# Performance work log

Hardware: AMD Instinct MI355X
Metric: run time of the kernel (lower is better)

## Reference

```python
import jax, jax.numpy as jnp
import numpy as np

NUM_HEADS = 4
OUTPUT_DIM = 64


def setup_inputs() -> dict:
    key = jax.random.key(0)
    k1, k2, k3 = jax.random.split(key, 3)
    B, N, F = 8, 2048, 256
    features = jax.random.normal(k1, (B, N, F), dtype=jnp.float32)
    adj_matrix = jax.random.uniform(k2, (B, N, N), dtype=jnp.float32)
    # learned params (glorot-ish scale)
    kernel = jax.random.normal(k3, (F, OUTPUT_DIM * NUM_HEADS), dtype=jnp.float32) * (1.0 / np.sqrt(F))
    bias = jnp.zeros((OUTPUT_DIM * NUM_HEADS,), dtype=jnp.float32)
    return {"features": features, "adj_matrix": adj_matrix, "kernel": kernel, "bias": bias}


def reference(features, adj_matrix, kernel, bias):
    B, N, F = features.shape
    H, D = NUM_HEADS, OUTPUT_DIM
    Wh = jnp.matmul(features, kernel)                 # [B, N, H*D]
    Whh = Wh.reshape(B, N, H, D)                      # [B, N, H, D]
    # per-node, per-head score: inner product Wh1 @ Wh2 = ||Wh||^2
    e = jnp.sum(Whh * Whh, axis=-1)                   # [B, N, H]
    attention = jax.nn.softmax(e, axis=1)             # softmax over nodes
    attention = jnp.mean(attention, axis=2)           # head mean -> [B, N]
    # adjacency mask (broadcast column score over neighbors)
    A = attention[:, :, None] * adj_matrix            # [B, N, N]
    out = jnp.matmul(A, Wh) + bias                    # [B, N, H*D]
    return jax.nn.relu(out)
```

## Files before the change

### kernel.cpp

```cpp
#include <hip/hip_runtime.h>
#include <hip/hip_bf16.h>

#define BATCH 8
#define NNODE 2048
#define FDIM 256
#define HD 256
#define NH 4
#define MROWS (BATCH*NNODE)

typedef float f32x4 __attribute__((ext_vector_type(4)));
typedef short s16x8 __attribute__((ext_vector_type(8)));
typedef unsigned short ushort_t;

#define MFMA __builtin_amdgcn_mfma_f32_16x16x32_bf16
#define SCHED0() __builtin_amdgcn_sched_barrier(0)
#define SBAR() __builtin_amdgcn_s_barrier()

__device__ __forceinline__ ushort_t f2bf(float f) {
    unsigned u = __builtin_bit_cast(unsigned, f);
    u += 0x7fffu + ((u >> 16) & 1u);
    return (ushort_t)(u >> 16);
}
__device__ __forceinline__ void split2(float f, ushort_t& h, ushort_t& l) {
    unsigned u = __builtin_bit_cast(unsigned, f);
    h = (ushort_t)(u >> 16);
    float fh = __builtin_bit_cast(float, u & 0xffff0000u);
    float lo = f - fh;
    l = (ushort_t)(__builtin_bit_cast(unsigned, lo) >> 16);
}

#define GLOAD16(gp, lp) __builtin_amdgcn_global_load_lds( \
    (const __attribute__((address_space(1))) void*)(gp),  \
    (__attribute__((address_space(3))) void*)(lp), 16, 0, 0)

__global__ __launch_bounds__(256) void wprep_kernel(
    const float* __restrict__ Wm,
    ushort_t* __restrict__ wt_hi, ushort_t* __restrict__ wt_lo)
{
    const int nn = blockIdx.x, k = threadIdx.x;
    ushort_t h, l;
    split2(Wm[(size_t)k * HD + nn], h, l);
    wt_hi[nn * FDIM + k] = h;
    wt_lo[nn * FDIM + k] = l;
}

__global__ __launch_bounds__(256, 4) void gemm1_kernel(
    const float* __restrict__ features,
    const ushort_t* __restrict__ wt_hi,
    const ushort_t* __restrict__ wt_lo,
    ushort_t* __restrict__ WhT_hi,
    ushort_t* __restrict__ WhT_lo,
    float* __restrict__ e_out)
{
    __shared__ __align__(16) ushort_t Ah[64 * 64];
    __shared__ __align__(16) ushort_t Al[64 * 64];
    __shared__ __align__(16) ushort_t Bh[64 * 64];
    __shared__ __align__(16) ushort_t Bl[64 * 64];
    __shared__ float red[64][2];

    const int tid = threadIdx.x, lane = tid & 63, w = tid >> 6;
    const int wr = w >> 1, wc = w & 1;
    const int row0 = blockIdx.x * 64;
    const int head = blockIdx.y;
    const int col0 = head * 64;

    const float* Ab = features + (size_t)row0 * FDIM;
    const ushort_t* Bhg = wt_hi + (size_t)col0 * FDIM;
    const ushort_t* Blg = wt_lo + (size_t)col0 * FDIM;

    const int sr0 = tid >> 3;
    const int sg8 = tid & 7;
    const int bc = (lane >> 3);
    const int bs = lane & 7;

    f32x4 ar[4];
    f32x4 acc[2][2];
    #pragma unroll
    for (int m = 0; m < 2; ++m)
        #pragma unroll
        for (int n = 0; n < 2; ++n) acc[m][n] = (f32x4)0.f;

    #define G1_LOADA(K0) do {                                                  \
        _Pragma("unroll")                                                      \
        for (int i = 0; i < 2; ++i) {                                          \
            const int r = sr0 + 32 * i;                                        \
            ar[2*i]   = *(const f32x4*)&Ab[(size_t)r * FDIM + (K0) + sg8 * 8]; \
            ar[2*i+1] = *(const f32x4*)&Ab[(size_t)r * FDIM + (K0) + sg8 * 8 + 4]; \
        }                                                                      \
    } while (0)

    #define G1_STAGEA() do {                                                   \
        _Pragma("unroll")                                                      \
        for (int i = 0; i < 2; ++i) {                                          \
            const int r = sr0 + 32 * i;                                        \
            s16x8 vh, vl; ushort_t hh, ll;                                     \
            _Pragma("unroll")                                                  \
            for (int j = 0; j < 4; ++j) {                                      \
                split2(ar[2*i][j], hh, ll);  vh[j] = (short)hh; vl[j] = (short)ll; \
            }                                                                  \
            _Pragma("unroll")                                                  \
            for (int j = 0; j < 4; ++j) {                                      \
                split2(ar[2*i+1][j], hh, ll); vh[4+j] = (short)hh; vl[4+j] = (short)ll; \
            }                                                                  \
            const int off = r * 64 + ((sg8 ^ (r & 7)) << 3);                   \
            *(s16x8*)&Ah[off] = vh; *(s16x8*)&Al[off] = vl;                    \
        }                                                                      \
    } while (0)

    #define G1_STAGEB(K0) do {                                                 \
        _Pragma("unroll")                                                      \
        for (int qq = 0; qq < 2; ++qq) {                                       \
            const int q = w + qq * 4;                                          \
            const int c = q * 8 + bc;                                          \
            const int g = bs ^ (c & 7);                                        \
            GLOAD16(&Bhg[(size_t)c * FDIM + (K0) + g * 8], &Bh[q * 512]);      \
            GLOAD16(&Blg[(size_t)c * FDIM + (K0) + g * 8], &Bl[q * 512]);      \
        }                                                                      \
    } while (0)

    G1_LOADA(0);
    for (int t = 0; t < 4; ++t) {
        G1_STAGEB(t * 64);
        G1_STAGEA();
        if (t < 3) G1_LOADA((t + 1) * 64);
        if (t < 3) { asm volatile("s_waitcnt lgkmcnt(0) vmcnt(4)" ::: "memory"); }
        else       { asm volatile("s_waitcnt lgkmcnt(0) vmcnt(0)" ::: "memory"); }
        SCHED0(); SBAR(); SCHED0();
        #pragma unroll
        for (int kh = 0; kh < 2; ++kh) {
            const int kg = kh * 4 + (lane >> 4);
            s16x8 afh[2], afl[2], bfh[2], bfl[2];
            #pragma unroll
            for (int m = 0; m < 2; ++m) {
                const int r = wr * 32 + m * 16 + (lane & 15);
                const int off = r * 64 + ((kg ^ (r & 7)) << 3);
                afh[m] = *(const s16x8*)&Ah[off];
                afl[m] = *(const s16x8*)&Al[off];
            }
            #pragma unroll
            for (int n = 0; n < 2; ++n) {
                const int c = wc * 32 + n * 16 + (lane & 15);
                const int off = c * 64 + ((kg ^ (c & 7)) << 3);
                bfh[n] = *(const s16x8*)&Bh[off];
                bfl[n] = *(const s16x8*)&Bl[off];
            }
            #pragma unroll
            for (int m = 0; m < 2; ++m)
                #pragma unroll
                for (int n = 0; n < 2; ++n) {
                    acc[m][n] = MFMA(afh[m], bfh[n], acc[m][n], 0, 0, 0);
                    acc[m][n] = MFMA(afh[m], bfl[n], acc[m][n], 0, 0, 0);
                    acc[m][n] = MFMA(afl[m], bfh[n], acc[m][n], 0, 0, 0);
                }
        }
        SCHED0(); SBAR(); SCHED0();
    }

    #pragma unroll
    for (int m = 0; m < 2; ++m)
        #pragma unroll
        for (int j = 0; j < 4; ++j) {
            float p = acc[m][0][j] * acc[m][0][j] + acc[m][1][j] * acc[m][1][j];
            p += __shfl_xor(p, 1, 64);
            p += __shfl_xor(p, 2, 64);
            p += __shfl_xor(p, 4, 64);
            p += __shfl_xor(p, 8, 64);
            if ((lane & 15) == 0)
                red[wr * 32 + m * 16 + (lane >> 4) * 4 + j][wc] = p;
        }

    __syncthreads();
    ushort_t* Th = Ah;
    ushort_t* Tl = Al;
    #pragma unroll
    for (int m = 0; m < 2; ++m)
        #pragma unroll
        for (int n = 0; n < 2; ++n)
            #pragma unroll
            for (int j = 0; j < 4; ++j) {
                const int rr = wr * 32 + m * 16 + (lane >> 4) * 4 + j;
                const int cc = wc * 32 + n * 16 + (lane & 15);
                const int ad = cc * 64 + ((((rr >> 3) ^ (cc & 7))) << 3) + (rr & 7);
                ushort_t hh, ll;
                split2(acc[m][n][j], hh, ll);
                Th[ad] = hh; Tl[ad] = ll;
            }
    __syncthreads();

    if (tid < 64) {
        const int rg = row0 + tid;
        e_out[((size_t)((rg >> 11) * NH + head)) * NNODE + (rg & 2047)] =
            red[tid][0] + red[tid][1];
    }
    const int bb = row0 >> 11, node0 = row0 & 2047;
    #pragma unroll
    for (int i = 0; i < 2; ++i) {
        const int gid = tid + 256 * i;
        const int c = gid >> 3, gr = gid & 7;
        const int ad = c * 64 + ((gr ^ (c & 7)) << 3);
        uint4 vh = *(const uint4*)&Th[ad];
        uint4 vl = *(const uint4*)&Tl[ad];
        const size_t o = ((size_t)bb * HD + col0 + c) * NNODE + node0 + gr * 8;
        *(uint4*)&WhT_hi[o] = vh;
        *(uint4*)&WhT_lo[o] = vl;
    }
}

__global__ __launch_bounds__(256) void sm_kernel(
    const float* __restrict__ e, float* __restrict__ ms)
{
    __shared__ float red[8];
    const int bh = blockIdx.x, tid = threadIdx.x;
    const int lane = tid & 63, w = tid >> 6;
    const float* row = e + (size_t)bh * NNODE;
    float mx = -3.0e38f;
    for (int n = tid; n < NNODE; n += 256) mx = fmaxf(mx, row[n]);
    #pragma unroll
    for (int off = 32; off; off >>= 1) mx = fmaxf(mx, __shfl_xor(mx, off, 64));
    if (lane == 0) red[w] = mx;
    __syncthreads();
    mx = fmaxf(fmaxf(red[0], red[1]), fmaxf(red[2], red[3]));
    float s = 0.f;
    for (int n = tid; n < NNODE; n += 256) s += expf(row[n] - mx);
    #pragma unroll
    for (int off = 32; off; off >>= 1) s += __shfl_xor(s, off, 64);
    if (lane == 0) red[4 + w] = s;
    __syncthreads();
    if (tid == 0) {
        ms[bh * 2] = mx;
        ms[bh * 2 + 1] = red[4] + red[5] + red[6] + red[7];
    }
}

__global__ __launch_bounds__(256) void att_kernel(
    const float* __restrict__ e, const float* __restrict__ ms,
    float* __restrict__ attv)
{
    const int i = blockIdx.x * 256 + threadIdx.x;
    const int b = i >> 11, n = i & 2047;
    float a = 0.f;
    #pragma unroll
    for (int h = 0; h < NH; ++h) {
        const int bh = b * NH + h;
        a += expf(e[(size_t)bh * NNODE + n] - ms[bh * 2]) / ms[bh * 2 + 1];
    }
    attv[i] = 0.25f * a;
}

__global__ __launch_bounds__(256, 2) void gemm2_kernel(
    const float* __restrict__ adj,
    const ushort_t* __restrict__ WhT_hi,
    const ushort_t* __restrict__ WhT_lo,
    const float* __restrict__ att,
    const float* __restrict__ bias,
    float* __restrict__ out)
{
    __shared__ __align__(16) ushort_t Bh[3][64 * 64];
    __shared__ __align__(16) ushort_t Bl[3][64 * 64];

    const int tid = threadIdx.x, lane = tid & 63, w = tid >> 6;

    const int bid = blockIdx.x;
    const int wg = (bid & 7) * 64 + (bid >> 3);
    const int bx = wg & 15, by = (wg >> 4) & 3, b = wg >> 6;
    const int row0 = bx * 128, col0 = by * 64;

    const ushort_t* Bhg = WhT_hi + ((size_t)b * HD + col0) * NNODE;
    const ushort_t* Blg = WhT_lo + ((size_t)b * HD + col0) * NNODE;

    const float* pA = adj + (size_t)b * NNODE * NNODE
                    + (size_t)(row0 + w * 32 + (lane & 15)) * NNODE
                    + ((lane >> 4) * 8);

    const int bc = lane >> 3, bs = lane & 7;

    f32x4 ar[2][2][2];
    s16x8 afh[2][2];
    f32x4 acc[2][4];
    #pragma unroll
    for (int m = 0; m < 2; ++m)
        #pragma unroll
        for (int n = 0; n < 4; ++n) acc[m][n] = (f32x4)0.f;

    #define G2_LOADA(K0) do {                                                   \
        _Pragma("unroll")                                                       \
        for (int m = 0; m < 2; ++m)                                             \
        _Pragma("unroll")                                                       \
        for (int ks = 0; ks < 2; ++ks) {                                        \
            ar[m][ks][0] = *(const f32x4*)&pA[(size_t)m * 16 * NNODE + (K0) + ks * 32]; \
            ar[m][ks][1] = *(const f32x4*)&pA[(size_t)m * 16 * NNODE + (K0) + ks * 32 + 4]; \
        }                                                                       \
    } while (0)

    #define G2_CONVERT() do {                                                   \
        _Pragma("unroll")                                                       \
        for (int m = 0; m < 2; ++m)                                             \
        _Pragma("unroll")                                                       \
        for (int ks = 0; ks < 2; ++ks)                                          \
        _Pragma("unroll")                                                       \
        for (int h2 = 0; h2 < 2; ++h2)                                          \
        _Pragma("unroll")                                                       \
        for (int j = 0; j < 4; ++j)                                             \
            afh[m][ks][h2 * 4 + j] = (short)f2bf(ar[m][ks][h2][j]);             \
    } while (0)

    #define G2_STAGEB(BUF, K0) do {                                             \
        _Pragma("unroll")                                                       \
        for (int qq = 0; qq < 2; ++qq) {                                        \
            const int q = w + qq * 4;                                           \
            const int c = q * 8 + bc;                                           \
            const int g = bs ^ (c & 7);                                         \
            GLOAD16(&Bhg[(size_t)c * NNODE + (K0) + g * 8], &Bh[BUF][q * 512]); \
            GLOAD16(&Blg[(size_t)c * NNODE + (K0) + g * 8], &Bl[BUF][q * 512]); \
        }                                                                       \
    } while (0)

    #define G2_COMPUTE(BHP, BLP) do {                                           \
        _Pragma("unroll")                                                       \
        for (int ks = 0; ks < 2; ++ks) {                                        \
            const int kg = ks * 4 + (lane >> 4);                                \
            s16x8 bfh[4], bfl[4];                                               \
            _Pragma("unroll")                                                   \
            for (int n = 0; n < 4; ++n) {                                       \
                const int c = n * 16 + (lane & 15);                             \
                const int off = c * 64 + ((kg ^ (c & 7)) << 3);                 \
                bfh[n] = *(const s16x8*)&(BHP)[off];                            \
                bfl[n] = *(const s16x8*)&(BLP)[off];                            \
            }                                                                   \
            __builtin_amdgcn_s_setprio(1);                                      \
            _Pragma("unroll")                                                   \
            for (int m = 0; m < 2; ++m)                                         \
            _Pragma("unroll")                                                   \
            for (int n = 0; n < 4; ++n)                                         \
                acc[m][n] = MFMA(afh[m][ks], bfh[n], acc[m][n], 0, 0, 0);       \
            _Pragma("unroll")                                                   \
            for (int m = 0; m < 2; ++m)                                         \
            _Pragma("unroll")                                                   \
            for (int n = 0; n < 4; ++n)                                         \
                acc[m][n] = MFMA(afh[m][ks], bfl[n], acc[m][n], 0, 0, 0);       \
            __builtin_amdgcn_s_setprio(0);                                      \
        }                                                                       \
    } while (0)

    G2_STAGEB(0, 0);
    G2_LOADA(0);

    int cur = 0;
    for (int t = 0; t < 32; ++t) {
        const int nxt = (cur == 2) ? 0 : cur + 1;
        if (t < 31) G2_STAGEB(nxt, (t + 1) * 64);
        G2_CONVERT();
        if (t < 31) G2_LOADA((t + 1) * 64);
        asm volatile("s_waitcnt vmcnt(12)" ::: "memory");
        SCHED0(); SBAR(); SCHED0();
        {
            const ushort_t* bhp = &Bh[cur][0];
            const ushort_t* blp = &Bl[cur][0];
            G2_COMPUTE(bhp, blp);
        }
        cur = nxt;
    }

    const float* attb = att + (size_t)b * NNODE;
    #pragma unroll
    for (int n = 0; n < 4; ++n) {
        const int c = col0 + n * 16 + (lane & 15);
        const float bv = bias[c];
        #pragma unroll
        for (int m = 0; m < 2; ++m)
            #pragma unroll
            for (int j = 0; j < 4; ++j) {
                const int row = row0 + w * 32 + m * 16 + (lane >> 4) * 4 + j;
                out[((size_t)b * NNODE + row) * HD + c] =
                    fmaxf(fmaf(acc[m][n][j], attb[row], bv), 0.f);
            }
    }
}

extern "C" void kernel_launch(void* const* d_in, const int* in_sizes, int n_in,
                              void* d_out, int out_size, void* d_ws, size_t ws_size,
                              hipStream_t stream) {
    const float* features = (const float*)d_in[0];
    const float* adj      = (const float*)d_in[1];
    const float* Wm       = (const float*)d_in[2];
    const float* bias     = (const float*)d_in[3];
    float* out = (float*)d_out;

    ushort_t* WhT_hi = (ushort_t*)d_ws;
    ushort_t* WhT_lo = WhT_hi + (size_t)BATCH * HD * NNODE;
    ushort_t* wt_hi  = WhT_lo + (size_t)BATCH * HD * NNODE;
    ushort_t* wt_lo  = wt_hi + FDIM * HD;
    float* e    = (float*)(wt_lo + FDIM * HD);
    float* ms   = e + (size_t)BATCH * NH * NNODE;
    float* attv = ms + 64;

    wprep_kernel<<<HD, 256, 0, stream>>>(Wm, wt_hi, wt_lo);
    gemm1_kernel<<<dim3(MROWS / 64, NH), 256, 0, stream>>>(
        features, wt_hi, wt_lo, WhT_hi, WhT_lo, e);
    sm_kernel<<<BATCH * NH, 256, 0, stream>>>(e, ms);
    att_kernel<<<MROWS / 256, 256, 0, stream>>>(e, ms, attv);
    gemm2_kernel<<<512, 256, 0, stream>>>(
        adj, WhT_hi, WhT_lo, attv, bias, out);
}
```

Baseline: 267.7 us.

## Drop bf16 lo-split for Wh in GEMM2, fuse attention into epilogue, deepen pipeline

```diff
diff --git a/kernel.cpp b/kernel.cpp
--- a/kernel.cpp
+++ b/kernel.cpp
@@ -49,7 +49,6 @@
     const ushort_t* __restrict__ wt_hi,
     const ushort_t* __restrict__ wt_lo,
     ushort_t* __restrict__ WhT_hi,
-    ushort_t* __restrict__ WhT_lo,
     float* __restrict__ e_out)
 {
     __shared__ __align__(16) ushort_t Ah[64 * 64];
@@ -171,7 +170,6 @@
 
     __syncthreads();
     ushort_t* Th = Ah;
-    ushort_t* Tl = Al;
     #pragma unroll
     for (int m = 0; m < 2; ++m)
         #pragma unroll
@@ -181,9 +179,7 @@
                 const int rr = wr * 32 + m * 16 + (lane >> 4) * 4 + j;
                 const int cc = wc * 32 + n * 16 + (lane & 15);
                 const int ad = cc * 64 + ((((rr >> 3) ^ (cc & 7))) << 3) + (rr & 7);
-                ushort_t hh, ll;
-                split2(acc[m][n][j], hh, ll);
-                Th[ad] = hh; Tl[ad] = ll;
+                Th[ad] = f2bf(acc[m][n][j]);
             }
     __syncthreads();
 
@@ -193,16 +189,17 @@
             red[tid][0] + red[tid][1];
     }
     const int bb = row0 >> 11, node0 = row0 & 2047;
-    #pragma unroll
-    for (int i = 0; i < 2; ++i) {
-        const int gid = tid + 256 * i;
-        const int c = gid >> 3, gr = gid & 7;
-        const int ad = c * 64 + ((gr ^ (c & 7)) << 3);
-        uint4 vh = *(const uint4*)&Th[ad];
-        uint4 vl = *(const uint4*)&Tl[ad];
-        const size_t o = ((size_t)bb * HD + col0 + c) * NNODE + node0 + gr * 8;
-        *(uint4*)&WhT_hi[o] = vh;
-        *(uint4*)&WhT_lo[o] = vl;
+    {
+        const int gid = tid + 256 * 0;
+        #pragma unroll
+        for (int i = 0; i < 2; ++i) {
+            const int g2 = gid + 256 * i;
+            const int c = g2 >> 3, gr = g2 & 7;
+            const int ad = c * 64 + ((gr ^ (c & 7)) << 3);
+            uint4 vh = *(const uint4*)&Th[ad];
+            const size_t o = ((size_t)bb * HD + col0 + c) * NNODE + node0 + gr * 8;
+            *(uint4*)&WhT_hi[o] = vh;
+        }
     }
 }
 
@@ -228,35 +225,19 @@
     __syncthreads();
     if (tid == 0) {
         ms[bh * 2] = mx;
-        ms[bh * 2 + 1] = red[4] + red[5] + red[6] + red[7];
-    }
-}
-
-__global__ __launch_bounds__(256) void att_kernel(
-    const float* __restrict__ e, const float* __restrict__ ms,
-    float* __restrict__ attv)
-{
-    const int i = blockIdx.x * 256 + threadIdx.x;
-    const int b = i >> 11, n = i & 2047;
-    float a = 0.f;
-    #pragma unroll
-    for (int h = 0; h < NH; ++h) {
-        const int bh = b * NH + h;
-        a += expf(e[(size_t)bh * NNODE + n] - ms[bh * 2]) / ms[bh * 2 + 1];
-    }
-    attv[i] = 0.25f * a;
+        ms[bh * 2 + 1] = 1.0f / (red[4] + red[5] + red[6] + red[7]);
+    }
 }
 
 __global__ __launch_bounds__(256, 2) void gemm2_kernel(
     const float* __restrict__ adj,
     const ushort_t* __restrict__ WhT_hi,
-    const ushort_t* __restrict__ WhT_lo,
-    const float* __restrict__ att,
+    const float* __restrict__ e,
+    const float* __restrict__ ms,
     const float* __restrict__ bias,
     float* __restrict__ out)
 {
-    __shared__ __align__(16) ushort_t Bh[3][64 * 64];
-    __shared__ __align__(16) ushort_t Bl[3][64 * 64];
+    __shared__ __align__(16) ushort_t Bh[4][64 * 64];
 
     const int tid = threadIdx.x, lane = tid & 63, w = tid >> 6;
 
@@ -266,15 +247,13 @@
     const int row0 = bx * 128, col0 = by * 64;
 
     const ushort_t* Bhg = WhT_hi + ((size_t)b * HD + col0) * NNODE;
-    const ushort_t* Blg = WhT_lo + ((size_t)b * HD + col0) * NNODE;
-
     const float* pA = adj + (size_t)b * NNODE * NNODE
                     + (size_t)(row0 + w * 32 + (lane & 15)) * NNODE
                     + ((lane >> 4) * 8);
 
     const int bc = lane >> 3, bs = lane & 7;
 
-    f32x4 ar[2][2][2];
+    f32x4 arE[8], arO[8];
     s16x8 afh[2][2];
     f32x4 acc[2][4];
     #pragma unroll
@@ -282,17 +261,17 @@
         #pragma unroll
         for (int n = 0; n < 4; ++n) acc[m][n] = (f32x4)0.f;
 
-    #define G2_LOADA(K0) do {                                                   \
+    #define G2_LOADA(AR, K0) do {                                               \
         _Pragma("unroll")                                                       \
         for (int m = 0; m < 2; ++m)                                             \
         _Pragma("unroll")                                                       \
         for (int ks = 0; ks < 2; ++ks) {                                        \
-            ar[m][ks][0] = *(const f32x4*)&pA[(size_t)m * 16 * NNODE + (K0) + ks * 32]; \
-            ar[m][ks][1] = *(const f32x4*)&pA[(size_t)m * 16 * NNODE + (K0) + ks * 32 + 4]; \
+            AR[m*4+ks*2+0] = *(const f32x4*)&pA[(size_t)m * 16 * NNODE + (K0) + ks * 32]; \
+            AR[m*4+ks*2+1] = *(const f32x4*)&pA[(size_t)m * 16 * NNODE + (K0) + ks * 32 + 4]; \
         }                                                                       \
     } while (0)
 
-    #define G2_CONVERT() do {                                                   \
+    #define G2_CONVERT(AR) do {                                                 \
         _Pragma("unroll")                                                       \
         for (int m = 0; m < 2; ++m)                                             \
         _Pragma("unroll")                                                       \
@@ -301,7 +280,7 @@
         for (int h2 = 0; h2 < 2; ++h2)                                          \
         _Pragma("unroll")                                                       \
         for (int j = 0; j < 4; ++j)                                             \
-            afh[m][ks][h2 * 4 + j] = (short)f2bf(ar[m][ks][h2][j]);             \
+            afh[m][ks][h2 * 4 + j] = (short)f2bf(AR[m*4+ks*2+h2][j]);           \
     } while (0)
 
     #define G2_STAGEB(BUF, K0) do {                                             \
@@ -311,21 +290,19 @@
             const int c = q * 8 + bc;                                           \
             const int g = bs ^ (c & 7);                                         \
             GLOAD16(&Bhg[(size_t)c * NNODE + (K0) + g * 8], &Bh[BUF][q * 512]); \
-            GLOAD16(&Blg[(size_t)c * NNODE + (K0) + g * 8], &Bl[BUF][q * 512]); \
         }                                                                       \
     } while (0)
 
-    #define G2_COMPUTE(BHP, BLP) do {                                           \
+    #define G2_COMPUTE(BUF) do {                                                \
         _Pragma("unroll")                                                       \
         for (int ks = 0; ks < 2; ++ks) {                                        \
             const int kg = ks * 4 + (lane >> 4);                                \
-            s16x8 bfh[4], bfl[4];                                               \
+            s16x8 bfh[4];                                                       \
             _Pragma("unroll")                                                   \
             for (int n = 0; n < 4; ++n) {                                       \
                 const int c = n * 16 + (lane & 15);                             \
                 const int off = c * 64 + ((kg ^ (c & 7)) << 3);                 \
-                bfh[n] = *(const s16x8*)&(BHP)[off];                            \
-                bfl[n] = *(const s16x8*)&(BLP)[off];                            \
+                bfh[n] = *(const s16x8*)&Bh[BUF][off];                          \
             }                                                                   \
             __builtin_amdgcn_s_setprio(1);                                      \
             _Pragma("unroll")                                                   \
@@ -333,35 +310,54 @@
             _Pragma("unroll")                                                   \
             for (int n = 0; n < 4; ++n)                                         \
                 acc[m][n] = MFMA(afh[m][ks], bfh[n], acc[m][n], 0, 0, 0);       \
-            _Pragma("unroll")                                                   \
-            for (int m = 0; m < 2; ++m)                                         \
-            _Pragma("unroll")                                                   \
-            for (int n = 0; n < 4; ++n)                                         \
-                acc[m][n] = MFMA(afh[m][ks], bfl[n], acc[m][n], 0, 0, 0);       \
             __builtin_amdgcn_s_setprio(0);                                      \
         }                                                                       \
     } while (0)
 
+    #define G2_TILE(AR, CBUF, SBUF, KC, DO_STAGE) do {                          \
+        if (DO_STAGE) G2_STAGEB(SBUF, (KC) + 128);                              \
+        G2_CONVERT(AR);                                                         \
+        if (DO_STAGE) G2_LOADA(AR, (KC) + 128);                                 \
+        asm volatile("s_waitcnt vmcnt(20)" ::: "memory");                       \
+        SCHED0(); SBAR(); SCHED0();                                             \
+        G2_COMPUTE(CBUF);                                                       \
+    } while (0)
+
     G2_STAGEB(0, 0);
-    G2_LOADA(0);
-
-    int cur = 0;
-    for (int t = 0; t < 32; ++t) {
-        const int nxt = (cur == 2) ? 0 : cur + 1;
-        if (t < 31) G2_STAGEB(nxt, (t + 1) * 64);
-        G2_CONVERT();
-        if (t < 31) G2_LOADA((t + 1) * 64);
-        asm volatile("s_waitcnt vmcnt(12)" ::: "memory");
-        SCHED0(); SBAR(); SCHED0();
-        {
-            const ushort_t* bhp = &Bh[cur][0];
-            const ushort_t* blp = &Bl[cur][0];
-            G2_COMPUTE(bhp, blp);
+    G2_LOADA(arE, 0);
+    G2_STAGEB(1, 64);
+    G2_LOADA(arO, 64);
+
+    #pragma unroll 1
+    for (int t = 0; t < 28; t += 4) {
+        G2_TILE(arE, 0, 2, t * 64, true);
+        G2_TILE(arO, 1, 3, (t + 1) * 64, true);
+        G2_TILE(arE, 2, 0, (t + 2) * 64, true);
+        G2_TILE(arO, 3, 1, (t + 3) * 64, true);
+    }
+    G2_TILE(arE, 0, 2, 28 * 64, true);
+    G2_TILE(arO, 1, 3, 29 * 64, true);
+    G2_TILE(arE, 2, 0, 30 * 64, false);
+    G2_TILE(arO, 3, 0, 31 * 64, false);
+
+    float msm[NH], msi[NH];
+    #pragma unroll
+    for (int h = 0; h < NH; ++h) {
+        msm[h] = ms[(b * NH + h) * 2];
+        msi[h] = ms[(b * NH + h) * 2 + 1];
+    }
+    float rowatt[2][4];
+    #pragma unroll
+    for (int m = 0; m < 2; ++m)
+        #pragma unroll
+        for (int j = 0; j < 4; ++j) {
+            const int row = row0 + w * 32 + m * 16 + (lane >> 4) * 4 + j;
+            float a = 0.f;
+            #pragma unroll
+            for (int h = 0; h < NH; ++h)
+                a += expf(e[((size_t)b * NH + h) * NNODE + row] - msm[h]) * msi[h];
+            rowatt[m][j] = 0.25f * a;
         }
-        cur = nxt;
-    }
-
-    const float* attb = att + (size_t)b * NNODE;
     #pragma unroll
     for (int n = 0; n < 4; ++n) {
         const int c = col0 + n * 16 + (lane & 15);
@@ -372,7 +368,7 @@
             for (int j = 0; j < 4; ++j) {
                 const int row = row0 + w * 32 + m * 16 + (lane >> 4) * 4 + j;
                 out[((size_t)b * NNODE + row) * HD + c] =
-                    fmaxf(fmaf(acc[m][n][j], attb[row], bv), 0.f);
+                    fmaxf(fmaf(acc[m][n][j], rowatt[m][j], bv), 0.f);
             }
     }
 }
@@ -387,18 +383,15 @@
     float* out = (float*)d_out;
 
     ushort_t* WhT_hi = (ushort_t*)d_ws;
-    ushort_t* WhT_lo = WhT_hi + (size_t)BATCH * HD * NNODE;
-    ushort_t* wt_hi  = WhT_lo + (size_t)BATCH * HD * NNODE;
+    ushort_t* wt_hi  = WhT_hi + (size_t)BATCH * HD * NNODE;
     ushort_t* wt_lo  = wt_hi + FDIM * HD;
-    float* e    = (float*)(wt_lo + FDIM * HD);
-    float* ms   = e + (size_t)BATCH * NH * NNODE;
-    float* attv = ms + 64;
+    float* e  = (float*)(wt_lo + FDIM * HD);
+    float* ms = e + (size_t)BATCH * NH * NNODE;
 
     wprep_kernel<<<HD, 256, 0, stream>>>(Wm, wt_hi, wt_lo);
     gemm1_kernel<<<dim3(MROWS / 64, NH), 256, 0, stream>>>(
-        features, wt_hi, wt_lo, WhT_hi, WhT_lo, e);
+        features, wt_hi, wt_lo, WhT_hi, e);
     sm_kernel<<<BATCH * NH, 256, 0, stream>>>(e, ms);
-    att_kernel<<<MROWS / 256, 256, 0, stream>>>(e, ms, attv);
     gemm2_kernel<<<512, 256, 0, stream>>>(
-        adj, WhT_hi, WhT_lo, attv, bias, out);
-}
+        adj, WhT_hi, e, ms, bias, out);
+}
```

Result: no change. 265.4 us (-0.9%).
